# Optimization experiments

Measured on AMD Instinct MI355X. Metric: run time of the kernel, lower is better.

Reference implementation:

```python
import jax, jax.numpy as jnp
import numpy as np

TAU = 0.5
EPS = 1e-8
NEG = -1e30  # masked logit value (finite to keep grads clean)

B, L1, L2 = 8, 2048, 2048


def setup_inputs() -> dict:
    key = jax.random.key(0)
    k1, k2 = jax.random.split(key)
    sim_matrix = jax.random.normal(k1, (B, L1, L2), dtype=jnp.float32)
    # per-sample valid lengths in [1024, 2048] so masking is exercised but no row is empty
    lengths = jax.random.randint(k2, (B, 2), 1024, 2049, dtype=jnp.int32)
    return {"sim_matrix": sim_matrix, "lengths": lengths}


def reference(sim_matrix, lengths):
    # mask[b,i,j] = (i < lengths[b,0]) & (j < lengths[b,1])
    i_idx = jnp.arange(sim_matrix.shape[1])[None, :, None]
    j_idx = jnp.arange(sim_matrix.shape[2])[None, None, :]
    mask = (i_idx < lengths[:, 0, None, None]) & (j_idx < lengths[:, 1, None, None])

    logits = jnp.where(mask, sim_matrix / TAU, NEG)
    row_sm = jax.nn.softmax(logits, axis=-1)   # competition over L2 per row
    col_sm = jax.nn.softmax(logits, axis=-2)   # competition over L1 per column

    # geometric mean of the two assignments; zero outside valid region
    out = jnp.where(mask, jnp.sqrt(EPS + row_sm * col_sm), 0.0)
    return out
```

## Files before the change

kernel.cpp:

```cpp
#include <hip/hip_runtime.h>
#include <math.h>

#define L 2048
#define BATCH 8
#define RPS 16
#define NSPLIT (L / RPS)
#define EPSF 1e-8f
#define C2 2.885390081777927f
#define C4 5.770780163555854f

typedef float f32x4 __attribute__((ext_vector_type(4)));

__device__ __forceinline__ float fexp2(float x) {
  return __builtin_amdgcn_exp2f(x);
}
__device__ __forceinline__ float fsqrt(float x) {
  return __builtin_amdgcn_sqrtf(x);
}

__global__ __launch_bounds__(256)
__attribute__((amdgpu_waves_per_eu(5, 5))) void stats_k(
    const float* __restrict__ sim, const int* __restrict__ lengths,
    float* __restrict__ rinv, float* __restrict__ pcol) {
  const int b = blockIdx.y;
  const int islab = blockIdx.x;
  const int len0 = lengths[2 * b], len1 = lengths[2 * b + 1];
  const int tid = threadIdx.x;
  const int wave = tid >> 6, lane = tid & 63;
  const int i0 = islab * RPS + wave * 4;
  const int jb = lane * 4;
  const int nrow = min(4, len0 - i0);

  float4 cacc[8];
#pragma unroll
  for (int s = 0; s < 8; ++s) cacc[s] = make_float4(0.f, 0.f, 0.f, 0.f);
  float racc[4] = {0.f, 0.f, 0.f, 0.f};

#pragma unroll
  for (int r = 0; r < 4; ++r) {
    if (r < nrow) {
      const float* p = sim + ((size_t)b * L + (i0 + r)) * L + jb;
      float acc = 0.f;
#pragma unroll
      for (int s = 0; s < 8; ++s) {
        float4 v = *reinterpret_cast<const float4*>(p + s * 256);
        float4 e;
        e.x = fexp2(v.x * C2); e.y = fexp2(v.y * C2);
        e.z = fexp2(v.z * C2); e.w = fexp2(v.w * C2);
        if (s >= 4) {
          const int j = s * 256 + jb;
          if (j + 0 >= len1) e.x = 0.f;
          if (j + 1 >= len1) e.y = 0.f;
          if (j + 2 >= len1) e.z = 0.f;
          if (j + 3 >= len1) e.w = 0.f;
        }
        acc += (e.x + e.y) + (e.z + e.w);
        cacc[s].x += e.x; cacc[s].y += e.y; cacc[s].z += e.z; cacc[s].w += e.w;
      }
      racc[r] = acc;
    }
  }

#pragma unroll
  for (int r = 0; r < 4; ++r) {
    float v = racc[r];
#pragma unroll
    for (int off = 1; off < 64; off <<= 1) v += __shfl_xor(v, off, 64);
    if (lane == 0 && r < nrow) rinv[(size_t)b * L + (i0 + r)] = 1.0f / v;
  }

  __shared__ float cpart[4][2048];
#pragma unroll
  for (int s = 0; s < 8; ++s)
    *reinterpret_cast<float4*>(&cpart[wave][s * 256 + jb]) = cacc[s];
  __syncthreads();

#pragma unroll
  for (int h = 0; h < 2; ++h) {
    const int c = h * 1024 + tid * 4;
    float4 a0 = *reinterpret_cast<const float4*>(&cpart[0][c]);
    float4 a1 = *reinterpret_cast<const float4*>(&cpart[1][c]);
    float4 a2 = *reinterpret_cast<const float4*>(&cpart[2][c]);
    float4 a3 = *reinterpret_cast<const float4*>(&cpart[3][c]);
    f32x4 o;
    o.x = (a0.x + a1.x) + (a2.x + a3.x);
    o.y = (a0.y + a1.y) + (a2.y + a3.y);
    o.z = (a0.z + a1.z) + (a2.z + a3.z);
    o.w = (a0.w + a1.w) + (a2.w + a3.w);
    __builtin_nontemporal_store(
        o, reinterpret_cast<f32x4*>(&pcol[(size_t)(b * NSPLIT + islab) * L + c]));
  }
}

__global__ __launch_bounds__(128) void col_merge_k(
    const float* __restrict__ pcol, float* __restrict__ cinv) {
  const int idx = blockIdx.x * 128 + threadIdx.x;
  const int b = idx >> 11, j = idx & (L - 1);
  const float* p = pcol + (size_t)b * NSPLIT * L + j;
  float s0 = 0.f, s1 = 0.f;
#pragma unroll 8
  for (int c = 0; c < NSPLIT; c += 2) {
    s0 += p[(size_t)c * L];
    s1 += p[(size_t)(c + 1) * L];
  }
  cinv[idx] = 1.0f / (s0 + s1);
}

__global__ __launch_bounds__(512) void finalize_k(
    const float* __restrict__ sim, const int* __restrict__ lengths,
    const float* __restrict__ rinv, const float* __restrict__ cinv,
    float* __restrict__ out) {
  const int row = blockIdx.x;
  const int b = row >> 11, i = row & (L - 1);
  const int len0 = lengths[2 * b], len1 = lengths[2 * b + 1];
  const int j = threadIdx.x * 4;
  const size_t off = (size_t)row * L + j;
  f32x4 o;
  if (i >= len0) {
    o = (f32x4){0.f, 0.f, 0.f, 0.f};
  } else {
    const float ri = rinv[row];
    f32x4 v = __builtin_nontemporal_load(
        reinterpret_cast<const f32x4*>(sim + off));
    f32x4 ci = *reinterpret_cast<const f32x4*>(cinv + ((size_t)b << 11) + j);
    o.x = (j + 0 < len1) ? fsqrt(EPSF + fexp2(v.x * C4) * ri * ci.x) : 0.f;
    o.y = (j + 1 < len1) ? fsqrt(EPSF + fexp2(v.y * C4) * ri * ci.y) : 0.f;
    o.z = (j + 2 < len1) ? fsqrt(EPSF + fexp2(v.z * C4) * ri * ci.z) : 0.f;
    o.w = (j + 3 < len1) ? fsqrt(EPSF + fexp2(v.w * C4) * ri * ci.w) : 0.f;
  }
  __builtin_nontemporal_store(o, reinterpret_cast<f32x4*>(out + off));
}

extern "C" void kernel_launch(void* const* d_in, const int* in_sizes, int n_in,
                              void* d_out, int out_size, void* d_ws, size_t ws_size,
                              hipStream_t stream) {
  const float* sim = (const float*)d_in[0];
  const int* lengths = (const int*)d_in[1];
  float* out = (float*)d_out;
  float* ws = (float*)d_ws;

  const int NR = BATCH * L;
  float* rinv = ws;
  float* cinv = ws + NR;
  float* pcol = ws + 2 * (size_t)NR;

  hipLaunchKernelGGL(stats_k, dim3(NSPLIT, BATCH), dim3(256), 0, stream,
                     sim, lengths, rinv, pcol);
  hipLaunchKernelGGL(col_merge_k, dim3(NR / 128), dim3(128), 0, stream,
                     pcol, cinv);
  hipLaunchKernelGGL(finalize_k, dim3(NR), dim3(512), 0, stream,
                     sim, lengths, rinv, cinv, out);
}
```

Baseline: 266.5 us.

## Double-buffer stats rows into LDS via async global_load_lds

Stats kernel now stages each row into a per-wave double-buffered LDS region using global_load_lds, prefetching the next row while computing exp sums on the current one, with manual vmcnt waits. The column-partial scratch reuses the same 64KB arena after a barrier, and the fixed waves-per-EU attribute is dropped. The aim is to hide global memory latency in the read-heavy stats pass. In exchange, 64KB of LDS per block limits occupancy, and the hand-written waitcnt counts must match the instructions the compiler actually emits.

After: 264.2 us. Within noise of the previous version (-0.9%).

```diff
diff --git a/kernel.cpp b/kernel.cpp
--- a/kernel.cpp
+++ b/kernel.cpp
@@ -10,6 +10,8 @@
 #define C4 5.770780163555854f
 
 typedef float f32x4 __attribute__((ext_vector_type(4)));
+typedef const __attribute__((address_space(1))) void GASV;
+typedef __attribute__((address_space(3))) void LASV;
 
 __device__ __forceinline__ float fexp2(float x) {
   return __builtin_amdgcn_exp2f(x);
@@ -18,8 +20,15 @@
   return __builtin_amdgcn_sqrtf(x);
 }
 
-__global__ __launch_bounds__(256)
-__attribute__((amdgpu_waves_per_eu(5, 5))) void stats_k(
+__device__ __forceinline__ void stage_row(const float* rowp, char* dst,
+                                          int lane) {
+#pragma unroll
+  for (int s = 0; s < 8; ++s)
+    __builtin_amdgcn_global_load_lds((GASV*)(rowp + s * 256 + lane * 4),
+                                     (LASV*)(dst + s * 1024), 16, 0, 0);
+}
+
+__global__ __launch_bounds__(256) void stats_k(
     const float* __restrict__ sim, const int* __restrict__ lengths,
     float* __restrict__ rinv, float* __restrict__ pcol) {
   const int b = blockIdx.y;
@@ -31,33 +40,49 @@
   const int jb = lane * 4;
   const int nrow = min(4, len0 - i0);
 
+  __shared__ char arena[65536];
+  char* mybuf = arena + (wave << 14);
+
   float4 cacc[8];
 #pragma unroll
   for (int s = 0; s < 8; ++s) cacc[s] = make_float4(0.f, 0.f, 0.f, 0.f);
   float racc[4] = {0.f, 0.f, 0.f, 0.f};
 
+  if (nrow > 0) {
+    const float* rbase = sim + ((size_t)b * L + i0) * L;
+    stage_row(rbase, mybuf, lane);
 #pragma unroll
-  for (int r = 0; r < 4; ++r) {
-    if (r < nrow) {
-      const float* p = sim + ((size_t)b * L + (i0 + r)) * L + jb;
-      float acc = 0.f;
+    for (int r = 0; r < 4; ++r) {
+      if (r < nrow) {
+        if (r + 1 < nrow) {
+          stage_row(rbase + (size_t)(r + 1) * L, mybuf + (((r + 1) & 1) << 13),
+                    lane);
+          asm volatile("s_waitcnt vmcnt(8)" ::: "memory");
+        } else {
+          asm volatile("s_waitcnt vmcnt(0)" ::: "memory");
+        }
+        __builtin_amdgcn_sched_barrier(0);
+        const char* cb = mybuf + ((r & 1) << 13);
+        float acc = 0.f;
 #pragma unroll
-      for (int s = 0; s < 8; ++s) {
-        float4 v = *reinterpret_cast<const float4*>(p + s * 256);
-        float4 e;
-        e.x = fexp2(v.x * C2); e.y = fexp2(v.y * C2);
-        e.z = fexp2(v.z * C2); e.w = fexp2(v.w * C2);
-        if (s >= 4) {
-          const int j = s * 256 + jb;
-          if (j + 0 >= len1) e.x = 0.f;
-          if (j + 1 >= len1) e.y = 0.f;
-          if (j + 2 >= len1) e.z = 0.f;
-          if (j + 3 >= len1) e.w = 0.f;
+        for (int s = 0; s < 8; ++s) {
+          f32x4 v = *reinterpret_cast<const f32x4*>(cb + s * 1024 + lane * 16);
+          float4 e;
+          e.x = fexp2(v.x * C2); e.y = fexp2(v.y * C2);
+          e.z = fexp2(v.z * C2); e.w = fexp2(v.w * C2);
+          if (s >= 4) {
+            const int j = s * 256 + jb;
+            if (j + 0 >= len1) e.x = 0.f;
+            if (j + 1 >= len1) e.y = 0.f;
+            if (j + 2 >= len1) e.z = 0.f;
+            if (j + 3 >= len1) e.w = 0.f;
+          }
+          acc += (e.x + e.y) + (e.z + e.w);
+          cacc[s].x += e.x; cacc[s].y += e.y;
+          cacc[s].z += e.z; cacc[s].w += e.w;
         }
-        acc += (e.x + e.y) + (e.z + e.w);
-        cacc[s].x += e.x; cacc[s].y += e.y; cacc[s].z += e.z; cacc[s].w += e.w;
+        racc[r] = acc;
       }
-      racc[r] = acc;
     }
   }
 
@@ -69,19 +94,20 @@
     if (lane == 0 && r < nrow) rinv[(size_t)b * L + (i0 + r)] = 1.0f / v;
   }
 
-  __shared__ float cpart[4][2048];
+  __syncthreads();
+  float* cp = reinterpret_cast<float*>(arena);
 #pragma unroll
   for (int s = 0; s < 8; ++s)
-    *reinterpret_cast<float4*>(&cpart[wave][s * 256 + jb]) = cacc[s];
+    *reinterpret_cast<float4*>(&cp[wave * 2048 + s * 256 + jb]) = cacc[s];
   __syncthreads();
 
 #pragma unroll
   for (int h = 0; h < 2; ++h) {
     const int c = h * 1024 + tid * 4;
-    float4 a0 = *reinterpret_cast<const float4*>(&cpart[0][c]);
-    float4 a1 = *reinterpret_cast<const float4*>(&cpart[1][c]);
-    float4 a2 = *reinterpret_cast<const float4*>(&cpart[2][c]);
-    float4 a3 = *reinterpret_cast<const float4*>(&cpart[3][c]);
+    float4 a0 = *reinterpret_cast<const float4*>(&cp[0 * 2048 + c]);
+    float4 a1 = *reinterpret_cast<const float4*>(&cp[1 * 2048 + c]);
+    float4 a2 = *reinterpret_cast<const float4*>(&cp[2 * 2048 + c]);
+    float4 a3 = *reinterpret_cast<const float4*>(&cp[3 * 2048 + c]);
     f32x4 o;
     o.x = (a0.x + a1.x) + (a2.x + a3.x);
     o.y = (a0.y + a1.y) + (a2.y + a3.y);
```
